# Kernel tuning notes

Hardware: AMD Instinct MI355X
Metric: run time of the kernel (lower is better)

The kernel has to match this reference:

```python
import jax, jax.numpy as jnp
import numpy as np

N_TOKENS = 16384
HIDDEN = 4096
N_EXPERTS = 64
TOP_K = 8


def setup_inputs() -> dict:
    key = jax.random.key(0)
    kx, kw, kb = jax.random.split(key, 3)
    x = jax.random.normal(kx, (N_TOKENS, HIDDEN), dtype=jnp.float32)
    # nn.Linear(hidden_dim, expert_num): weight [E, H], bias [E]
    W = jax.random.normal(kw, (N_EXPERTS, HIDDEN), dtype=jnp.float32) * (1.0 / np.sqrt(HIDDEN))
    b = jax.random.normal(kb, (N_EXPERTS,), dtype=jnp.float32) * 0.01
    return {"x": x, "W": W, "b": b}


def reference(x, W, b):
    # gate linear: [N, H] @ [H, E] + [E] -> [N, E]
    router = jnp.einsum("nh,eh->ne", x, W) + b
    # softmax over experts
    router_logits = jax.nn.softmax(router, axis=-1)
    # top-k over experts: values/indices [N, K]
    top_k_logits, top_k_indices = jax.lax.top_k(router_logits, TOP_K)
    # renormalize the selected probs
    router_weight = top_k_logits / jnp.sum(top_k_logits, axis=-1, keepdims=True)
    router_weight = router_weight.astype(x.dtype)
    # one-hot mask [N, K, E] -> permute(2,1,0) -> [E, K, N]
    expert_mask = jax.nn.one_hot(top_k_indices, N_EXPERTS, dtype=jnp.int32)
    expert_mask = jnp.transpose(expert_mask, (2, 1, 0))
    return (router, router_weight, top_k_indices, expert_mask)
```

## Files before the change

### kernel.cpp

```cpp
#include <hip/hip_runtime.h>

#define N_TOK 16384
#define HID   4096
#define N_EXP 64
#define TOPK  8

#define SPLIT  4
#define KSLICE (HID / SPLIT)
#define CH     32
#define NCH    (KSLICE / CH)
#define LSTR   68

#define OFF_WT   (N_TOK * N_EXP)
#define OFF_IDX  (OFF_WT + N_TOK * TOPK)
#define OFF_MASK (OFF_IDX + N_TOK * TOPK)

__global__ __launch_bounds__(256, 4)
void router_gemm(const float* __restrict__ x, const float* __restrict__ W,
                 float* __restrict__ router)
{
    __shared__ float xs[2][CH][LSTR];
    __shared__ float ws[2][CH][LSTR];

    const int tid = threadIdx.x;
    const int tb  = blockIdx.x & 255;
    const int ks  = blockIdx.x >> 8;
    const long t0 = (long)tb * 64;
    const int h0  = ks * KSLICE;

    const int lane = tid & 63;
    const int wv   = tid >> 6;
    const int eg   = lane & 15;
    const int tg   = lane >> 4;
    const int trow = wv * 16 + tg * 4;
    const int ecol = eg * 4;

    const int tf = tid >> 3;
    const int hq = tid & 7;

    const float* xsrc = x + (t0 + tf) * (long)HID + h0 + 4 * hq;
    const float* wsrc = W + (long)tf * HID + h0 + 4 * hq;

    float acc[4][4] = {{0.f}};

    float4 px0 = *(const float4*)(xsrc);
    float4 px1 = *(const float4*)(xsrc + 32 * (long)HID);
    float4 pw0 = *(const float4*)(wsrc);
    float4 pw1 = *(const float4*)(wsrc + 32 * (long)HID);

#pragma unroll
    for (int j = 0; j < 4; ++j) {
        xs[0][4 * hq + j][tf]      = ((const float*)&px0)[j];
        xs[0][4 * hq + j][tf + 32] = ((const float*)&px1)[j];
        ws[0][4 * hq + j][tf]      = ((const float*)&pw0)[j];
        ws[0][4 * hq + j][tf + 32] = ((const float*)&pw1)[j];
    }
    __syncthreads();

    for (int c = 0; c < NCH; ++c) {
        const int buf = c & 1;

        if (c + 1 < NCH) {
            const float* xn = xsrc + (c + 1) * CH;
            const float* wn = wsrc + (c + 1) * CH;
            px0 = *(const float4*)(xn);
            px1 = *(const float4*)(xn + 32 * (long)HID);
            pw0 = *(const float4*)(wn);
            pw1 = *(const float4*)(wn + 32 * (long)HID);
        }

#pragma unroll 4
        for (int k = 0; k < CH; ++k) {
            float4 xq = *(const float4*)&xs[buf][k][trow];
            float4 wq = *(const float4*)&ws[buf][k][ecol];
            acc[0][0] = fmaf(xq.x, wq.x, acc[0][0]);
            acc[0][1] = fmaf(xq.x, wq.y, acc[0][1]);
            acc[0][2] = fmaf(xq.x, wq.z, acc[0][2]);
            acc[0][3] = fmaf(xq.x, wq.w, acc[0][3]);
            acc[1][0] = fmaf(xq.y, wq.x, acc[1][0]);
            acc[1][1] = fmaf(xq.y, wq.y, acc[1][1]);
            acc[1][2] = fmaf(xq.y, wq.z, acc[1][2]);
            acc[1][3] = fmaf(xq.y, wq.w, acc[1][3]);
            acc[2][0] = fmaf(xq.z, wq.x, acc[2][0]);
            acc[2][1] = fmaf(xq.z, wq.y, acc[2][1]);
            acc[2][2] = fmaf(xq.z, wq.z, acc[2][2]);
            acc[2][3] = fmaf(xq.z, wq.w, acc[2][3]);
            acc[3][0] = fmaf(xq.w, wq.x, acc[3][0]);
            acc[3][1] = fmaf(xq.w, wq.y, acc[3][1]);
            acc[3][2] = fmaf(xq.w, wq.z, acc[3][2]);
            acc[3][3] = fmaf(xq.w, wq.w, acc[3][3]);
        }

        if (c + 1 < NCH) {
            const int nb = buf ^ 1;
#pragma unroll
            for (int j = 0; j < 4; ++j) {
                xs[nb][4 * hq + j][tf]      = ((const float*)&px0)[j];
                xs[nb][4 * hq + j][tf + 32] = ((const float*)&px1)[j];
                ws[nb][4 * hq + j][tf]      = ((const float*)&pw0)[j];
                ws[nb][4 * hq + j][tf + 32] = ((const float*)&pw1)[j];
            }
        }
        __syncthreads();
    }

    float* rbase = router + (t0 + trow) * (long)N_EXP + ecol;
#pragma unroll
    for (int i = 0; i < 4; ++i)
#pragma unroll
        for (int j = 0; j < 4; ++j)
            unsafeAtomicAdd(rbase + (long)i * N_EXP + j, acc[i][j]);
}

__global__ __launch_bounds__(256)
void router_topk(float* __restrict__ router, const float* __restrict__ b,
                 float* __restrict__ out)
{
    const int tid  = threadIdx.x;
    const int lane = tid & 63;
    const int wv   = tid >> 6;
    const int n    = blockIdx.x * 4 + wv;

    float l = router[(long)n * N_EXP + lane] + b[lane];
    router[(long)n * N_EXP + lane] = l;

    float m = l;
#pragma unroll
    for (int o = 32; o > 0; o >>= 1) m = fmaxf(m, __shfl_xor(m, o));
    float p = expf(l - m);
    float Z = p;
#pragma unroll
    for (int o = 32; o > 0; o >>= 1) Z += __shfl_xor(Z, o);
    float prob = p / Z;

    float cur = prob;
    float myv = 0.f;
    int   myi = 0;
    float ssum = 0.f;
#pragma unroll
    for (int k = 0; k < TOPK; ++k) {
        float v = cur;
        int   id = lane;
#pragma unroll
        for (int o = 32; o > 0; o >>= 1) {
            float ov = __shfl_xor(v, o);
            int   oi = __shfl_xor(id, o);
            if (ov > v || (ov == v && oi < id)) { v = ov; id = oi; }
        }
        if (lane == k)  { myv = v; myi = id; }
        if (lane == id) cur = -1.f;
        ssum += v;
    }

    if (lane < TOPK) {
        out[OFF_WT  + (long)n * TOPK + lane] = myv / ssum;
        out[OFF_IDX + (long)n * TOPK + lane] = (float)myi;
        out[OFF_MASK + (long)myi * (TOPK * N_TOK) + (long)lane * N_TOK + n] = 1.0f;
    }
}

extern "C" void kernel_launch(void* const* d_in, const int* in_sizes, int n_in,
                              void* d_out, int out_size, void* d_ws, size_t ws_size,
                              hipStream_t stream)
{
    const float* x = (const float*)d_in[0];
    const float* W = (const float*)d_in[1];
    const float* b = (const float*)d_in[2];
    float* out = (float*)d_out;

    hipMemsetAsync(out, 0, (size_t)out_size * sizeof(float), stream);

    hipLaunchKernelGGL(router_gemm, dim3(256 * SPLIT), dim3(256), 0, stream,
                       x, W, out);
    hipLaunchKernelGGL(router_topk, dim3(N_TOK / 4), dim3(256), 0, stream,
                       out, b, out);
}
```

Measured before the change: 448.6 us.

## Use split-fp16 MFMA for router GEMM and write mask densely instead of memset

Replaces the scalar FP32 FMA GEMM with MFMA 16x16x32 fp16 instructions. Each fp32 operand is split into high and low fp16 parts, and three products are summed to keep near-fp32 accuracy. W is pre-split by a small prep kernel into the workspace. The split-K atomics and the full-output memset are removed, so each block now covers all of K and adds the bias itself. The one-hot mask is written densely by a new kernel, which also zeroes it. The trade-offs are extra kernel launches, fp16 range and precision risk, and only 256 blocks, which may underfill the GPU.

```diff
diff --git a/kernel.cpp b/kernel.cpp
--- a/kernel.cpp
+++ b/kernel.cpp
@@ -5,124 +5,161 @@
 #define N_EXP 64
 #define TOPK  8
 
-#define SPLIT  4
-#define KSLICE (HID / SPLIT)
-#define CH     32
-#define NCH    (KSLICE / CH)
-#define LSTR   68
+#define CH    64
+#define NST   (HID / CH)
 
 #define OFF_WT   (N_TOK * N_EXP)
 #define OFF_IDX  (OFF_WT + N_TOK * TOPK)
 #define OFF_MASK (OFF_IDX + N_TOK * TOPK)
 
-__global__ __launch_bounds__(256, 4)
-void router_gemm(const float* __restrict__ x, const float* __restrict__ W,
+typedef __attribute__((ext_vector_type(8))) _Float16 f16x8;
+typedef __attribute__((ext_vector_type(4))) float f32x4;
+
+static __device__ __forceinline__ void hsplit(float f, unsigned short &h, unsigned short &l)
+{
+    _Float16 hh = (_Float16)f;
+    float r = f - (float)hh;
+    _Float16 hl = (_Float16)r;
+    h = __builtin_bit_cast(unsigned short, hh);
+    l = __builtin_bit_cast(unsigned short, hl);
+}
+
+__global__ __launch_bounds__(256)
+void prep_w(const float* __restrict__ W,
+            unsigned short* __restrict__ wh, unsigned short* __restrict__ wl)
+{
+    const int i = blockIdx.x * 256 + threadIdx.x;
+    float4 f = ((const float4*)W)[i];
+    unsigned short h0,l0,h1,l1,h2,l2,h3,l3;
+    hsplit(f.x,h0,l0); hsplit(f.y,h1,l1); hsplit(f.z,h2,l2); hsplit(f.w,h3,l3);
+    *(uint2*)&wh[4*i] = make_uint2((unsigned)h0 | ((unsigned)h1<<16), (unsigned)h2 | ((unsigned)h3<<16));
+    *(uint2*)&wl[4*i] = make_uint2((unsigned)l0 | ((unsigned)l1<<16), (unsigned)l2 | ((unsigned)l3<<16));
+}
+
+__global__ __launch_bounds__(256, 1)
+void router_gemm(const float* __restrict__ x,
+                 const unsigned short* __restrict__ wh,
+                 const unsigned short* __restrict__ wl,
+                 const float* __restrict__ b,
                  float* __restrict__ router)
 {
-    __shared__ float xs[2][CH][LSTR];
-    __shared__ float ws[2][CH][LSTR];
+    __shared__ unsigned short sXh[2][64 * CH];
+    __shared__ unsigned short sXl[2][64 * CH];
+    __shared__ unsigned short sWh[2][64 * CH];
+    __shared__ unsigned short sWl[2][64 * CH];
 
     const int tid = threadIdx.x;
-    const int tb  = blockIdx.x & 255;
-    const int ks  = blockIdx.x >> 8;
-    const long t0 = (long)tb * 64;
-    const int h0  = ks * KSLICE;
-
-    const int lane = tid & 63;
-    const int wv   = tid >> 6;
-    const int eg   = lane & 15;
-    const int tg   = lane >> 4;
-    const int trow = wv * 16 + tg * 4;
-    const int ecol = eg * 4;
-
-    const int tf = tid >> 3;
-    const int hq = tid & 7;
-
-    const float* xsrc = x + (t0 + tf) * (long)HID + h0 + 4 * hq;
-    const float* wsrc = W + (long)tf * HID + h0 + 4 * hq;
-
-    float acc[4][4] = {{0.f}};
-
-    float4 px0 = *(const float4*)(xsrc);
-    float4 px1 = *(const float4*)(xsrc + 32 * (long)HID);
-    float4 pw0 = *(const float4*)(wsrc);
-    float4 pw1 = *(const float4*)(wsrc + 32 * (long)HID);
-
-#pragma unroll
-    for (int j = 0; j < 4; ++j) {
-        xs[0][4 * hq + j][tf]      = ((const float*)&px0)[j];
-        xs[0][4 * hq + j][tf + 32] = ((const float*)&px1)[j];
-        ws[0][4 * hq + j][tf]      = ((const float*)&pw0)[j];
-        ws[0][4 * hq + j][tf + 32] = ((const float*)&pw1)[j];
-    }
+    const long t0 = (long)blockIdx.x * 64;
+
+    const int xr0 = tid >> 4, xkq = tid & 15;
+    const int wr0 = tid >> 3, wq  = tid & 7;
+
+    const float*          xb  = x  + (t0 + xr0) * (long)HID + xkq * 4;
+    const unsigned short* whb = wh + (long)wr0 * HID + wq * 8;
+    const unsigned short* wlb = wl + (long)wr0 * HID + wq * 8;
+
+    const int lane = tid & 63, wv = tid >> 6;
+    const int wr = wv >> 1, wc = wv & 1;
+    const int lrow = lane & 15, lg = lane >> 4, sw = lane & 7;
+
+    float4 gx[4]; uint4 gwh[2], gwl[2];
+    f32x4 acc[2][2] = {};
+
+    auto LOAD = [&](int st) {
+        const long o = (long)st * CH;
+#pragma unroll
+        for (int j = 0; j < 4; ++j)
+            gx[j] = *(const float4*)(xb + (long)(16 * j) * HID + o);
+#pragma unroll
+        for (int j = 0; j < 2; ++j) {
+            gwh[j] = *(const uint4*)(whb + (long)(32 * j) * HID + o);
+            gwl[j] = *(const uint4*)(wlb + (long)(32 * j) * HID + o);
+        }
+    };
+
+    auto STORE = [&](int buf) {
+#pragma unroll
+        for (int j = 0; j < 4; ++j) {
+            const int r = xr0 + 16 * j;
+            const int q = xkq >> 1;
+            const int a = r * CH + (((q ^ (r & 7)) << 3) | ((xkq & 1) << 2));
+            unsigned short h0,l0,h1,l1,h2,l2,h3,l3;
+            hsplit(gx[j].x,h0,l0); hsplit(gx[j].y,h1,l1);
+            hsplit(gx[j].z,h2,l2); hsplit(gx[j].w,h3,l3);
+            *(uint2*)&sXh[buf][a] = make_uint2((unsigned)h0 | ((unsigned)h1<<16), (unsigned)h2 | ((unsigned)h3<<16));
+            *(uint2*)&sXl[buf][a] = make_uint2((unsigned)l0 | ((unsigned)l1<<16), (unsigned)l2 | ((unsigned)l3<<16));
+        }
+#pragma unroll
+        for (int j = 0; j < 2; ++j) {
+            const int r = wr0 + 32 * j;
+            const int a = r * CH + ((wq ^ (r & 7)) << 3);
+            *(uint4*)&sWh[buf][a] = gwh[j];
+            *(uint4*)&sWl[buf][a] = gwl[j];
+        }
+    };
+
+    auto COMPUTE = [&](int buf) {
+#pragma unroll
+        for (int ks = 0; ks < CH / 32; ++ks) {
+            f16x8 ah[2], al[2], bh[2], bl[2];
+            const int qs = ((ks * 4 + lg) ^ sw) << 3;
+#pragma unroll
+            for (int ti = 0; ti < 2; ++ti) {
+                const int a = (wr * 32 + ti * 16 + lrow) * CH + qs;
+                ah[ti] = *(const f16x8*)&sXh[buf][a];
+                al[ti] = *(const f16x8*)&sXl[buf][a];
+            }
+#pragma unroll
+            for (int ei = 0; ei < 2; ++ei) {
+                const int a = (wc * 32 + ei * 16 + lrow) * CH + qs;
+                bh[ei] = *(const f16x8*)&sWh[buf][a];
+                bl[ei] = *(const f16x8*)&sWl[buf][a];
+            }
+#pragma unroll
+            for (int ti = 0; ti < 2; ++ti)
+#pragma unroll
+                for (int ei = 0; ei < 2; ++ei) {
+                    acc[ti][ei] = __builtin_amdgcn_mfma_f32_16x16x32_f16(ah[ti], bh[ei], acc[ti][ei], 0, 0, 0);
+                    acc[ti][ei] = __builtin_amdgcn_mfma_f32_16x16x32_f16(ah[ti], bl[ei], acc[ti][ei], 0, 0, 0);
+                    acc[ti][ei] = __builtin_amdgcn_mfma_f32_16x16x32_f16(al[ti], bh[ei], acc[ti][ei], 0, 0, 0);
+                }
+        }
+    };
+
+    LOAD(0);
+    STORE(0);
     __syncthreads();
-
-    for (int c = 0; c < NCH; ++c) {
-        const int buf = c & 1;
-
-        if (c + 1 < NCH) {
-            const float* xn = xsrc + (c + 1) * CH;
-            const float* wn = wsrc + (c + 1) * CH;
-            px0 = *(const float4*)(xn);
-            px1 = *(const float4*)(xn + 32 * (long)HID);
-            pw0 = *(const float4*)(wn);
-            pw1 = *(const float4*)(wn + 32 * (long)HID);
-        }
-
-#pragma unroll 4
-        for (int k = 0; k < CH; ++k) {
-            float4 xq = *(const float4*)&xs[buf][k][trow];
-            float4 wq = *(const float4*)&ws[buf][k][ecol];
-            acc[0][0] = fmaf(xq.x, wq.x, acc[0][0]);
-            acc[0][1] = fmaf(xq.x, wq.y, acc[0][1]);
-            acc[0][2] = fmaf(xq.x, wq.z, acc[0][2]);
-            acc[0][3] = fmaf(xq.x, wq.w, acc[0][3]);
-            acc[1][0] = fmaf(xq.y, wq.x, acc[1][0]);
-            acc[1][1] = fmaf(xq.y, wq.y, acc[1][1]);
-            acc[1][2] = fmaf(xq.y, wq.z, acc[1][2]);
-            acc[1][3] = fmaf(xq.y, wq.w, acc[1][3]);
-            acc[2][0] = fmaf(xq.z, wq.x, acc[2][0]);
-            acc[2][1] = fmaf(xq.z, wq.y, acc[2][1]);
-            acc[2][2] = fmaf(xq.z, wq.z, acc[2][2]);
-            acc[2][3] = fmaf(xq.z, wq.w, acc[2][3]);
-            acc[3][0] = fmaf(xq.w, wq.x, acc[3][0]);
-            acc[3][1] = fmaf(xq.w, wq.y, acc[3][1]);
-            acc[3][2] = fmaf(xq.w, wq.z, acc[3][2]);
-            acc[3][3] = fmaf(xq.w, wq.w, acc[3][3]);
-        }
-
-        if (c + 1 < NCH) {
-            const int nb = buf ^ 1;
-#pragma unroll
-            for (int j = 0; j < 4; ++j) {
-                xs[nb][4 * hq + j][tf]      = ((const float*)&px0)[j];
-                xs[nb][4 * hq + j][tf + 32] = ((const float*)&px1)[j];
-                ws[nb][4 * hq + j][tf]      = ((const float*)&pw0)[j];
-                ws[nb][4 * hq + j][tf + 32] = ((const float*)&pw1)[j];
+#pragma unroll 1
+    for (int st = 0; st < NST; ++st) {
+        if (st + 1 < NST) LOAD(st + 1);
+        COMPUTE(st & 1);
+        if (st + 1 < NST) STORE((st + 1) & 1);
+        __syncthreads();
+    }
+
+#pragma unroll
+    for (int ei = 0; ei < 2; ++ei) {
+        const int e = wc * 32 + ei * 16 + lrow;
+        const float bias = b[e];
+#pragma unroll
+        for (int ti = 0; ti < 2; ++ti)
+#pragma unroll
+            for (int r = 0; r < 4; ++r) {
+                const long tok = t0 + wr * 32 + ti * 16 + lg * 4 + r;
+                router[tok * N_EXP + e] = acc[ti][ei][r] + bias;
             }
-        }
-        __syncthreads();
-    }
-
-    float* rbase = router + (t0 + trow) * (long)N_EXP + ecol;
-#pragma unroll
-    for (int i = 0; i < 4; ++i)
-#pragma unroll
-        for (int j = 0; j < 4; ++j)
-            unsafeAtomicAdd(rbase + (long)i * N_EXP + j, acc[i][j]);
+    }
 }
 
 __global__ __launch_bounds__(256)
-void router_topk(float* __restrict__ router, const float* __restrict__ b,
-                 float* __restrict__ out)
+void router_topk(const float* __restrict__ router, float* __restrict__ out)
 {
     const int tid  = threadIdx.x;
     const int lane = tid & 63;
     const int wv   = tid >> 6;
     const int n    = blockIdx.x * 4 + wv;
 
-    float l = router[(long)n * N_EXP + lane] + b[lane];
-    router[(long)n * N_EXP + lane] = l;
+    float l = router[(long)n * N_EXP + lane];
 
     float m = l;
 #pragma unroll
@@ -155,7 +192,26 @@
     if (lane < TOPK) {
         out[OFF_WT  + (long)n * TOPK + lane] = myv / ssum;
         out[OFF_IDX + (long)n * TOPK + lane] = (float)myi;
-        out[OFF_MASK + (long)myi * (TOPK * N_TOK) + (long)lane * N_TOK + n] = 1.0f;
+    }
+}
+
+__global__ __launch_bounds__(256)
+void mask_fill(const float* __restrict__ idxf, float* __restrict__ mask)
+{
+    const int bid = blockIdx.x;
+    const int ek  = bid >> 2, qtr = bid & 3;
+    const int k   = ek & 7;
+    const float fe = (float)(ek >> 3);
+    float* mbase = mask + (long)ek * N_TOK;
+#pragma unroll
+    for (int j = 0; j < 4; ++j) {
+        const int n = qtr * 4096 + j * 1024 + threadIdx.x * 4;
+        float4 v;
+        v.x = (idxf[(long)(n + 0) * TOPK + k] == fe) ? 1.f : 0.f;
+        v.y = (idxf[(long)(n + 1) * TOPK + k] == fe) ? 1.f : 0.f;
+        v.z = (idxf[(long)(n + 2) * TOPK + k] == fe) ? 1.f : 0.f;
+        v.w = (idxf[(long)(n + 3) * TOPK + k] == fe) ? 1.f : 0.f;
+        *(float4*)&mbase[n] = v;
     }
 }
 
@@ -168,10 +224,12 @@
     const float* b = (const float*)d_in[2];
     float* out = (float*)d_out;
 
-    hipMemsetAsync(out, 0, (size_t)out_size * sizeof(float), stream);
-
-    hipLaunchKernelGGL(router_gemm, dim3(256 * SPLIT), dim3(256), 0, stream,
-                       x, W, out);
-    hipLaunchKernelGGL(router_topk, dim3(N_TOK / 4), dim3(256), 0, stream,
-                       out, b, out);
-}
+    unsigned short* wsh = (unsigned short*)d_ws;
+    unsigned short* wsl = wsh + (size_t)N_EXP * HID;
+
+    hipLaunchKernelGGL(prep_w,      dim3(N_EXP * HID / 1024), dim3(256), 0, stream, W, wsh, wsl);
+    hipLaunchKernelGGL(router_gemm, dim3(N_TOK / 64),         dim3(256), 0, stream, x, wsh, wsl, b, out);
+    hipLaunchKernelGGL(router_topk, dim3(N_TOK / 4),          dim3(256), 0, stream, out, out);
+    hipLaunchKernelGGL(mask_fill,   dim3(N_EXP * TOPK * 4),   dim3(256), 0, stream,
+                       out + OFF_IDX, out + OFF_MASK);
+}
```

Result: slower. 460.0 us (+2.5%).
